# Kernel tuning notes

Hardware: AMD Instinct MI355X
Metric: run time of the kernel (lower is better)

## Reference

```python
import jax, jax.numpy as jnp
import numpy as np

B, T, IN = 128, 512, 3          # batch, stroke seq len, (dx,dy,pen)
A, H = 77, 512                  # alphabet size, hidden size
KW, KM, U = 10, 20, 64          # window mixtures, MDN mixtures, char seq len
OUT = 6 * KM + 1                # MDN output size


def setup_inputs() -> dict:
    key = jax.random.key(0)
    ks = jax.random.split(key, 16)
    p = lambda k, *sh: (jax.random.normal(k, sh, jnp.float32) * 0.05)
    in1 = IN + A            # lstm1 input: [x_t, w_prev]
    in2 = IN + A + H        # lstm2 input: [x_t, w_t, h1]
    return dict(
        x=jax.random.normal(ks[0], (B, T, IN), jnp.float32),
        c_seq=jax.random.uniform(ks[1], (B, U, A), jnp.float32),
        Wih1=p(ks[2], 4 * H, in1), Whh1=p(ks[3], 4 * H, H),
        bih1=p(ks[4], 4 * H), bhh1=p(ks[5], 4 * H),
        Wih2=p(ks[6], 4 * H, in2), Whh2=p(ks[7], 4 * H, H),
        bih2=p(ks[8], 4 * H), bhh2=p(ks[9], 4 * H),
        W_abk=p(ks[10], 3 * KW, H), b_abk=p(ks[11], 3 * KW),
        W_fc2=p(ks[12], OUT, H), b_fc2=p(ks[13], OUT),
    )


def _lstm_cell(xt, h, c, Wih, Whh, bih, bhh):
    # torch gate order: i, f, g, o
    z = xt @ Wih.T + h @ Whh.T + bih + bhh
    i, f, g, o = jnp.split(z, 4, axis=-1)
    c_new = jax.nn.sigmoid(f) * c + jax.nn.sigmoid(i) * jnp.tanh(g)
    h_new = jax.nn.sigmoid(o) * jnp.tanh(c_new)
    return h_new, c_new


def reference(x, c_seq, Wih1, Whh1, bih1, bhh1, Wih2, Whh2, bih2, bhh2,
              W_abk, b_abk, W_fc2, b_fc2):
    Bsz = x.shape[0]
    u = jnp.arange(c_seq.shape[1], dtype=jnp.float32)  # [U]

    def step(carry, x_t):
        h1, c1, h2, c2, kappa, w_pre = carry
        # first LSTM on [x_t, w_{t-1}]
        h1, c1 = _lstm_cell(jnp.concatenate([x_t, w_pre], -1), h1, c1,
                            Wih1, Whh1, bih1, bhh1)
        # attention window params
        abk = h1 @ W_abk.T + b_abk
        a_hat, b_hat, k_hat = jnp.split(abk, 3, axis=-1)
        alpha, beta = jnp.exp(a_hat), jnp.exp(b_hat)
        kappa = kappa + jnp.exp(k_hat)
        # phi[b,u] = sum_k alpha * exp(-beta * (kappa - u)^2)
        phi = jnp.sum(alpha[:, None, :] *
                      jnp.exp(-beta[:, None, :] *
                              (kappa[:, None, :] - u[None, :, None]) ** 2),
                      axis=2)                      # [B, U]
        w_t = jnp.einsum('bu,bua->ba', phi, c_seq)  # [B, A]
        # second LSTM on [x_t, w_t, h1]
        h2, c2 = _lstm_cell(jnp.concatenate([x_t, w_t, h1], -1), h2, c2,
                            Wih2, Whh2, bih2, bhh2)
        out = h2 @ W_fc2.T + b_fc2                  # [B, OUT]
        return (h1, c1, h2, c2, kappa, w_t), out

    z = lambda *sh: jnp.zeros(sh, x.dtype)
    carry0 = (z(Bsz, H), z(Bsz, H), z(Bsz, H), z(Bsz, H),
              z(Bsz, KW), z(Bsz, A))
    _, outs = jax.lax.scan(step, carry0, jnp.swapaxes(x, 0, 1))
    outs = jnp.swapaxes(outs, 0, 1)                 # [B, T, OUT]

    # MixtureDensityLayer
    K = KM
    pi = jax.nn.softmax(outs[..., :K], axis=-1)
    mu1 = outs[..., K:2 * K]
    mu2 = outs[..., 2 * K:3 * K]
    std1 = jnp.exp(outs[..., 3 * K:4 * K])
    std2 = jnp.exp(outs[..., 4 * K:5 * K])
    corr = jnp.tanh(outs[..., 5 * K:6 * K])
    eot = jax.nn.sigmoid(outs[..., -1:])
    return (pi, mu1, mu2, std1, std2, corr, eot)
```

## Files before the change

kernel.cpp:

```cpp
#include <hip/hip_runtime.h>
#include <math.h>

#define BB   128
#define TT   512
#define INX  3
#define AA   77
#define HH   512
#define KWD  10
#define KMD  20
#define UU   64
#define OUTD 121
#define IN1  80
#define IN2  592

#define MT   8
#define NJ   16
#define GRT  (HH/NJ)
#define MTL  (BB/MT)

#define PC1  596
#define PC3  1108

#define BH   (BB*HH)
#define BA   (BB*AA)
#define BKW  (BB*KWD)

__device__ __forceinline__ float sigf(float x) { return 1.0f / (1.0f + expf(-x)); }

__device__ __forceinline__ float dot4(float4 w, float4 a) {
    return w.x * a.x + w.y * a.y + w.z * a.z + w.w * a.w;
}

__device__ __forceinline__ void fc2_post(const float* __restrict__ h2r,
                                         const float* __restrict__ W_fc2,
                                         const float* __restrict__ b_fc2,
                                         float* __restrict__ out,
                                         int brow, int tprev, int tid,
                                         float* sY, float* sRed)
{
    if (tid < OUTD) {
        const float4* wr = (const float4*)(W_fc2 + (size_t)tid * HH);
        const float4* hv = (const float4*)h2r;
        float acc = b_fc2[tid];
#pragma unroll 4
        for (int k = 0; k < HH / 4; ++k)
            acc += dot4(wr[k], hv[k]);
        sY[tid] = acc;
    }
    __syncthreads();
    if (tid == 0) {
        float mx = sY[0];
        for (int i = 1; i < KMD; ++i) mx = fmaxf(mx, sY[i]);
        float s = 0.f;
        for (int i = 0; i < KMD; ++i) s += expf(sY[i] - mx);
        sRed[0] = mx; sRed[1] = s;
    }
    __syncthreads();
    if (tid < OUTD) {
        const size_t SZ = (size_t)BB * TT * KMD;
        const size_t bt = (size_t)brow * TT + tprev;
        float y = sY[tid];
        if      (tid <     KMD) out[             bt * KMD + tid          ] = expf(y - sRed[0]) / sRed[1];
        else if (tid < 2 * KMD) out[    SZ +     bt * KMD + (tid -   KMD)] = y;
        else if (tid < 3 * KMD) out[2 * SZ +     bt * KMD + (tid - 2*KMD)] = y;
        else if (tid < 4 * KMD) out[3 * SZ +     bt * KMD + (tid - 3*KMD)] = expf(y);
        else if (tid < 5 * KMD) out[4 * SZ +     bt * KMD + (tid - 4*KMD)] = expf(y);
        else if (tid < 6 * KMD) out[5 * SZ +     bt * KMD + (tid - 5*KMD)] = tanhf(y);
        else                    out[6 * SZ + bt] = sigf(y);
    }
}

__global__ __launch_bounds__(512, 4) void k1(
    const float* __restrict__ x,
    const float* __restrict__ Wih1, const float* __restrict__ Whh1,
    const float* __restrict__ bih1, const float* __restrict__ bhh1,
    const float* __restrict__ W_fc2, const float* __restrict__ b_fc2,
    const float* __restrict__ h1_old, float* __restrict__ h1_new,
    float* __restrict__ c1,
    const float* __restrict__ w_pre, const float* __restrict__ h2_prev,
    float* __restrict__ out, int t)
{
    __shared__ float sCat[MT][PC1];
    __shared__ float sZp[4][MT][68];
    __shared__ float sY[OUTD];
    __shared__ float sRed[2];

    const int tid  = threadIdx.x;
    const int grt  = blockIdx.x;
    const int mtl  = blockIdx.y;
    const int row0 = mtl * MT, unit0 = grt * NJ;

    {
        const int r = tid >> 6, c = tid & 63;
        const int b = row0 + r;
        const float4* s1 = (const float4*)(h1_old + (size_t)b * HH);
        float4* d1 = (float4*)&sCat[r][IN1];
        for (int i = c; i < HH / 4; i += 64) d1[i] = s1[i];
        for (int i = c; i < IN1; i += 64)
            sCat[r][i] = (i < INX) ? x[((size_t)b * TT + t) * INX + i]
                                   : w_pre[(size_t)b * AA + (i - INX)];
    }
    __syncthreads();

    {
        const int m = tid & 7, j = (tid >> 3) & 15, kq = tid >> 7;
        const int i0 = kq * 37, i1 = i0 + 37;
        const int u = unit0 + j;
        float a0 = 0.f, a1 = 0.f, a2 = 0.f, a3 = 0.f;
        const float4* sc = (const float4*)&sCat[m][0];

        const float4* w0a = (const float4*)Wih1 + (size_t)u * 20;
        const float4* w1a = (const float4*)Wih1 + (size_t)(HH + u) * 20;
        const float4* w2a = (const float4*)Wih1 + (size_t)(2 * HH + u) * 20;
        const float4* w3a = (const float4*)Wih1 + (size_t)(3 * HH + u) * 20;
        const int aEnd = (i1 < 20) ? i1 : 20;
        for (int i = i0; i < aEnd; ++i) {
            float4 a = sc[i];
            a0 += dot4(w0a[i], a); a1 += dot4(w1a[i], a);
            a2 += dot4(w2a[i], a); a3 += dot4(w3a[i], a);
        }
        const float4* w0b = (const float4*)Whh1 + (size_t)u * 128;
        const float4* w1b = (const float4*)Whh1 + (size_t)(HH + u) * 128;
        const float4* w2b = (const float4*)Whh1 + (size_t)(2 * HH + u) * 128;
        const float4* w3b = (const float4*)Whh1 + (size_t)(3 * HH + u) * 128;
        const int bSt = (i0 > 20) ? i0 : 20;
#pragma unroll 4
        for (int i = bSt; i < i1; ++i) {
            float4 a = sc[i];
            const int k = i - 20;
            a0 += dot4(w0b[k], a); a1 += dot4(w1b[k], a);
            a2 += dot4(w2b[k], a); a3 += dot4(w3b[k], a);
        }
        sZp[kq][m][j]      = a0;
        sZp[kq][m][16 + j] = a1;
        sZp[kq][m][32 + j] = a2;
        sZp[kq][m][48 + j] = a3;
    }
    __syncthreads();

    if (tid < MT * NJ) {
        const int m = tid >> 4, j = tid & 15;
        const int u = unit0 + j;
        float z[4];
#pragma unroll
        for (int g = 0; g < 4; ++g) {
            const int wr = g * HH + u;
            z[g] = bih1[wr] + bhh1[wr]
                 + sZp[0][m][g * 16 + j] + sZp[1][m][g * 16 + j]
                 + sZp[2][m][g * 16 + j] + sZp[3][m][g * 16 + j];
        }
        const size_t gi = (size_t)(row0 + m) * HH + u;
        const float cold = c1[gi];
        const float cn = sigf(z[1]) * cold + sigf(z[0]) * tanhf(z[2]);
        c1[gi] = cn;
        h1_new[gi] = sigf(z[3]) * tanhf(cn);
    }

    if (t > 0 && grt < MT) {
        const int brow = row0 + grt;
        fc2_post(h2_prev + (size_t)brow * HH, W_fc2, b_fc2, out, brow, t - 1, tid, sY, sRed);
    }
}

__global__ __launch_bounds__(256) void k2(
    const float* __restrict__ c_seq,
    const float* __restrict__ W_abk, const float* __restrict__ b_abk,
    const float* __restrict__ h1_cur,
    const float* __restrict__ kap_old, float* __restrict__ kap_new,
    float* __restrict__ w_new)
{
    __shared__ float sH1[HH];
    __shared__ float sAbk[32];
    __shared__ float sAl[KWD], sBe[KWD], sKa[KWD];
    __shared__ float sPhi[UU];

    const int tid = threadIdx.x;
    const int b   = blockIdx.x;

    if (tid < HH / 4)
        ((float4*)sH1)[tid] = ((const float4*)(h1_cur + (size_t)b * HH))[tid];
    __syncthreads();

    {
        const int o = tid >> 3, kk = tid & 7;
        float acc = 0.f;
        if (o < 3 * KWD) {
            const float4* wp = (const float4*)(W_abk + (size_t)o * HH) + kk * 16;
            const float4* hp = (const float4*)sH1 + kk * 16;
#pragma unroll
            for (int k = 0; k < 16; ++k)
                acc += dot4(wp[k], hp[k]);
        }
        acc += __shfl_xor(acc, 1);
        acc += __shfl_xor(acc, 2);
        acc += __shfl_xor(acc, 4);
        if (o < 3 * KWD && kk == 0) sAbk[o] = acc + b_abk[o];
    }
    __syncthreads();

    if (tid < KWD) {
        const float al = expf(sAbk[tid]);
        const float be = expf(sAbk[KWD + tid]);
        const float ka = kap_old[(size_t)b * KWD + tid] + expf(sAbk[2 * KWD + tid]);
        sAl[tid] = al; sBe[tid] = be; sKa[tid] = ka;
        kap_new[(size_t)b * KWD + tid] = ka;
    }
    __syncthreads();

    if (tid < UU) {
        const float u = (float)tid;
        float s = 0.f;
#pragma unroll
        for (int k = 0; k < KWD; ++k) {
            const float d = sKa[k] - u;
            s += sAl[k] * expf(-sBe[k] * d * d);
        }
        sPhi[tid] = s;
    }
    __syncthreads();

    if (tid < AA) {
        float s = 0.f;
        const float* cp = c_seq + (size_t)b * UU * AA + tid;
#pragma unroll 4
        for (int u = 0; u < UU; ++u) s += sPhi[u] * cp[(size_t)u * AA];
        w_new[(size_t)b * AA + tid] = s;
    }
}

__global__ __launch_bounds__(512, 4) void k3(
    const float* __restrict__ x,
    const float* __restrict__ Wih2, const float* __restrict__ Whh2,
    const float* __restrict__ bih2, const float* __restrict__ bhh2,
    const float* __restrict__ h1_cur, const float* __restrict__ w_cur,
    const float* __restrict__ h2_old, float* __restrict__ h2_new,
    float* __restrict__ c2, int t)
{
    __shared__ float sCat[MT][PC3];
    __shared__ float sZp[4][MT][68];

    const int tid  = threadIdx.x;
    const int grt  = blockIdx.x;
    const int mtl  = blockIdx.y;
    const int row0 = mtl * MT, unit0 = grt * NJ;

    {
        const int r = tid >> 6, c = tid & 63;
        const int b = row0 + r;
        const float4* s1 = (const float4*)(h1_cur + (size_t)b * HH);
        const float4* s2 = (const float4*)(h2_old + (size_t)b * HH);
        float4* d1 = (float4*)&sCat[r][IN1];
        float4* d2 = (float4*)&sCat[r][IN2];
        for (int i = c; i < HH / 4; i += 64) { d1[i] = s1[i]; d2[i] = s2[i]; }
        for (int i = c; i < IN1; i += 64)
            sCat[r][i] = (i < INX) ? x[((size_t)b * TT + t) * INX + i]
                                   : w_cur[(size_t)b * AA + (i - INX)];
    }
    __syncthreads();

    {
        const int m = tid & 7, j = (tid >> 3) & 15, kq = tid >> 7;
        const int i0 = kq * 69, i1 = i0 + 69;
        const int u = unit0 + j;
        float a0 = 0.f, a1 = 0.f, a2 = 0.f, a3 = 0.f;
        const float4* sc = (const float4*)&sCat[m][0];

        const float4* w0a = (const float4*)Wih2 + (size_t)u * 148;
        const float4* w1a = (const float4*)Wih2 + (size_t)(HH + u) * 148;
        const float4* w2a = (const float4*)Wih2 + (size_t)(2 * HH + u) * 148;
        const float4* w3a = (const float4*)Wih2 + (size_t)(3 * HH + u) * 148;
        const int aEnd = (i1 < 148) ? i1 : 148;
#pragma unroll 4
        for (int i = i0; i < aEnd; ++i) {
            float4 a = sc[i];
            a0 += dot4(w0a[i], a); a1 += dot4(w1a[i], a);
            a2 += dot4(w2a[i], a); a3 += dot4(w3a[i], a);
        }
        const float4* w0b = (const float4*)Whh2 + (size_t)u * 128;
        const float4* w1b = (const float4*)Whh2 + (size_t)(HH + u) * 128;
        const float4* w2b = (const float4*)Whh2 + (size_t)(2 * HH + u) * 128;
        const float4* w3b = (const float4*)Whh2 + (size_t)(3 * HH + u) * 128;
        const int bSt = (i0 > 148) ? i0 : 148;
#pragma unroll 4
        for (int i = bSt; i < i1; ++i) {
            float4 a = sc[i];
            const int k = i - 148;
            a0 += dot4(w0b[k], a); a1 += dot4(w1b[k], a);
            a2 += dot4(w2b[k], a); a3 += dot4(w3b[k], a);
        }
        sZp[kq][m][j]      = a0;
        sZp[kq][m][16 + j] = a1;
        sZp[kq][m][32 + j] = a2;
        sZp[kq][m][48 + j] = a3;
    }
    __syncthreads();

    if (tid < MT * NJ) {
        const int m = tid >> 4, j = tid & 15;
        const int u = unit0 + j;
        float z[4];
#pragma unroll
        for (int g = 0; g < 4; ++g) {
            const int wr = g * HH + u;
            z[g] = bih2[wr] + bhh2[wr]
                 + sZp[0][m][g * 16 + j] + sZp[1][m][g * 16 + j]
                 + sZp[2][m][g * 16 + j] + sZp[3][m][g * 16 + j];
        }
        const size_t gi = (size_t)(row0 + m) * HH + u;
        const float cold = c2[gi];
        const float cn = sigf(z[1]) * cold + sigf(z[0]) * tanhf(z[2]);
        c2[gi] = cn;
        h2_new[gi] = sigf(z[3]) * tanhf(cn);
    }
}

__global__ __launch_bounds__(128) void fc2_final(
    const float* __restrict__ h2_last,
    const float* __restrict__ W_fc2, const float* __restrict__ b_fc2,
    float* __restrict__ out)
{
    __shared__ float sY[OUTD];
    __shared__ float sRed[2];
    const int brow = blockIdx.x;
    fc2_post(h2_last + (size_t)brow * HH, W_fc2, b_fc2, out, brow, TT - 1, threadIdx.x, sY, sRed);
}

extern "C" void kernel_launch(void* const* d_in, const int* in_sizes, int n_in,
                              void* d_out, int out_size, void* d_ws, size_t ws_size,
                              hipStream_t stream) {
    const float* x     = (const float*)d_in[0];
    const float* c_seq = (const float*)d_in[1];
    const float* Wih1  = (const float*)d_in[2];
    const float* Whh1  = (const float*)d_in[3];
    const float* bih1  = (const float*)d_in[4];
    const float* bhh1  = (const float*)d_in[5];
    const float* Wih2  = (const float*)d_in[6];
    const float* Whh2  = (const float*)d_in[7];
    const float* bih2  = (const float*)d_in[8];
    const float* bhh2  = (const float*)d_in[9];
    const float* W_abk = (const float*)d_in[10];
    const float* b_abk = (const float*)d_in[11];
    const float* W_fc2 = (const float*)d_in[12];
    const float* b_fc2 = (const float*)d_in[13];
    float* out = (float*)d_out;

    float* ws  = (float*)d_ws;
    float* h1b = ws;
    float* h2b = ws + 2 * BH;
    float* c1  = ws + 4 * BH;
    float* c2  = ws + 5 * BH;
    float* kap = ws + 6 * BH;
    float* wb  = ws + 6 * BH + 2 * BKW;
    const size_t used = (size_t)6 * BH + 2 * BKW + 2 * BA;

    hipMemsetAsync(d_ws, 0, used * sizeof(float), stream);

    const dim3 grid(GRT, MTL), blk(512);
    for (int t = 0; t < TT; ++t) {
        const int p = t & 1;
        k1<<<grid, blk, 0, stream>>>(x, Wih1, Whh1, bih1, bhh1, W_fc2, b_fc2,
                                     h1b + (size_t)p * BH, h1b + (size_t)(1 - p) * BH, c1,
                                     wb + (size_t)p * BA, h2b + (size_t)p * BH, out, t);
        k2<<<dim3(BB), dim3(256), 0, stream>>>(c_seq, W_abk, b_abk,
                                               h1b + (size_t)(1 - p) * BH,
                                               kap + (size_t)p * BKW, kap + (size_t)(1 - p) * BKW,
                                               wb + (size_t)(1 - p) * BA);
        k3<<<grid, blk, 0, stream>>>(x, Wih2, Whh2, bih2, bhh2,
                                     h1b + (size_t)(1 - p) * BH, wb + (size_t)(1 - p) * BA,
                                     h2b + (size_t)p * BH, h2b + (size_t)(1 - p) * BH, c2, t);
    }
    fc2_final<<<dim3(BB), dim3(128), 0, stream>>>(h2b, W_fc2, b_fc2, out);
}
```

Measured before the change: 43.82 ms.

## Fuse per-timestep LSTM kernels into one persistent cooperative kernel with grid syncs

Replaces the three kernel launches per timestep (LSTM1, attention, LSTM2) with a single cooperative persistent kernel. It loops over all timesteps and separates the phases with grid-wide syncs, which removes about 1500 kernel launches and their launch gaps. Work-groups shrink from 512 to 256 threads, each splitting the K reduction two ways instead of four, so two groups can sit on each CU. If the cooperative launch fails, it falls back to the multi-launch path. The cost is grid-barrier latency and lower per-group parallelism in the gate matvecs.

```diff
diff --git a/kernel.cpp b/kernel.cpp
--- a/kernel.cpp
+++ b/kernel.cpp
@@ -1,5 +1,8 @@
 #include <hip/hip_runtime.h>
+#include <hip/hip_cooperative_groups.h>
 #include <math.h>
+
+namespace cg = cooperative_groups;
 
 #define BB   128
 #define TT   512
@@ -17,6 +20,7 @@
 #define NJ   16
 #define GRT  (HH/NJ)
 #define MTL  (BB/MT)
+#define NWG  (GRT*MTL)
 
 #define PC1  596
 #define PC3  1108
@@ -70,44 +74,33 @@
     }
 }
 
-__global__ __launch_bounds__(512, 4) void k1(
+__device__ __forceinline__ void lstm1_body(
     const float* __restrict__ x,
     const float* __restrict__ Wih1, const float* __restrict__ Whh1,
     const float* __restrict__ bih1, const float* __restrict__ bhh1,
-    const float* __restrict__ W_fc2, const float* __restrict__ b_fc2,
     const float* __restrict__ h1_old, float* __restrict__ h1_new,
-    float* __restrict__ c1,
-    const float* __restrict__ w_pre, const float* __restrict__ h2_prev,
-    float* __restrict__ out, int t)
-{
-    __shared__ float sCat[MT][PC1];
-    __shared__ float sZp[4][MT][68];
-    __shared__ float sY[OUTD];
-    __shared__ float sRed[2];
-
-    const int tid  = threadIdx.x;
-    const int grt  = blockIdx.x;
-    const int mtl  = blockIdx.y;
+    float* __restrict__ c1, const float* __restrict__ w_pre,
+    int t, int tid, int grt, int mtl, float* sCat, float* sZp)
+{
     const int row0 = mtl * MT, unit0 = grt * NJ;
-
     {
-        const int r = tid >> 6, c = tid & 63;
+        const int r = tid >> 5, cc = tid & 31;
         const int b = row0 + r;
+        float* rowp = sCat + r * PC1;
         const float4* s1 = (const float4*)(h1_old + (size_t)b * HH);
-        float4* d1 = (float4*)&sCat[r][IN1];
-        for (int i = c; i < HH / 4; i += 64) d1[i] = s1[i];
-        for (int i = c; i < IN1; i += 64)
-            sCat[r][i] = (i < INX) ? x[((size_t)b * TT + t) * INX + i]
-                                   : w_pre[(size_t)b * AA + (i - INX)];
-    }
-    __syncthreads();
-
+        float4* d1 = (float4*)(rowp + IN1);
+        for (int i = cc; i < HH / 4; i += 32) d1[i] = s1[i];
+        for (int i = cc; i < IN1; i += 32)
+            rowp[i] = (i < INX) ? x[((size_t)b * TT + t) * INX + i]
+                                : w_pre[(size_t)b * AA + (i - INX)];
+    }
+    __syncthreads();
     {
         const int m = tid & 7, j = (tid >> 3) & 15, kq = tid >> 7;
-        const int i0 = kq * 37, i1 = i0 + 37;
+        const int i0 = kq * 74, i1 = i0 + 74;
         const int u = unit0 + j;
         float a0 = 0.f, a1 = 0.f, a2 = 0.f, a3 = 0.f;
-        const float4* sc = (const float4*)&sCat[m][0];
+        const float4* sc = (const float4*)(sCat + m * PC1);
 
         const float4* w0a = (const float4*)Wih1 + (size_t)u * 20;
         const float4* w1a = (const float4*)Wih1 + (size_t)(HH + u) * 20;
@@ -131,23 +124,23 @@
             a0 += dot4(w0b[k], a); a1 += dot4(w1b[k], a);
             a2 += dot4(w2b[k], a); a3 += dot4(w3b[k], a);
         }
-        sZp[kq][m][j]      = a0;
-        sZp[kq][m][16 + j] = a1;
-        sZp[kq][m][32 + j] = a2;
-        sZp[kq][m][48 + j] = a3;
-    }
-    __syncthreads();
-
+        float* zr = sZp + ((kq << 3) | m) * 68;
+        zr[j]      = a0;
+        zr[16 + j] = a1;
+        zr[32 + j] = a2;
+        zr[48 + j] = a3;
+    }
+    __syncthreads();
     if (tid < MT * NJ) {
         const int m = tid >> 4, j = tid & 15;
         const int u = unit0 + j;
+        const float* z0 = sZp + m * 68;
+        const float* z1 = sZp + (8 + m) * 68;
         float z[4];
 #pragma unroll
         for (int g = 0; g < 4; ++g) {
             const int wr = g * HH + u;
-            z[g] = bih1[wr] + bhh1[wr]
-                 + sZp[0][m][g * 16 + j] + sZp[1][m][g * 16 + j]
-                 + sZp[2][m][g * 16 + j] + sZp[3][m][g * 16 + j];
+            z[g] = bih1[wr] + bhh1[wr] + z0[g * 16 + j] + z1[g * 16 + j];
         }
         const size_t gi = (size_t)(row0 + m) * HH + u;
         const float cold = c1[gi];
@@ -155,115 +148,38 @@
         c1[gi] = cn;
         h1_new[gi] = sigf(z[3]) * tanhf(cn);
     }
-
-    if (t > 0 && grt < MT) {
-        const int brow = row0 + grt;
-        fc2_post(h2_prev + (size_t)brow * HH, W_fc2, b_fc2, out, brow, t - 1, tid, sY, sRed);
-    }
-}
-
-__global__ __launch_bounds__(256) void k2(
-    const float* __restrict__ c_seq,
-    const float* __restrict__ W_abk, const float* __restrict__ b_abk,
-    const float* __restrict__ h1_cur,
-    const float* __restrict__ kap_old, float* __restrict__ kap_new,
-    float* __restrict__ w_new)
-{
-    __shared__ float sH1[HH];
-    __shared__ float sAbk[32];
-    __shared__ float sAl[KWD], sBe[KWD], sKa[KWD];
-    __shared__ float sPhi[UU];
-
-    const int tid = threadIdx.x;
-    const int b   = blockIdx.x;
-
-    if (tid < HH / 4)
-        ((float4*)sH1)[tid] = ((const float4*)(h1_cur + (size_t)b * HH))[tid];
-    __syncthreads();
-
-    {
-        const int o = tid >> 3, kk = tid & 7;
-        float acc = 0.f;
-        if (o < 3 * KWD) {
-            const float4* wp = (const float4*)(W_abk + (size_t)o * HH) + kk * 16;
-            const float4* hp = (const float4*)sH1 + kk * 16;
-#pragma unroll
-            for (int k = 0; k < 16; ++k)
-                acc += dot4(wp[k], hp[k]);
-        }
-        acc += __shfl_xor(acc, 1);
-        acc += __shfl_xor(acc, 2);
-        acc += __shfl_xor(acc, 4);
-        if (o < 3 * KWD && kk == 0) sAbk[o] = acc + b_abk[o];
-    }
-    __syncthreads();
-
-    if (tid < KWD) {
-        const float al = expf(sAbk[tid]);
-        const float be = expf(sAbk[KWD + tid]);
-        const float ka = kap_old[(size_t)b * KWD + tid] + expf(sAbk[2 * KWD + tid]);
-        sAl[tid] = al; sBe[tid] = be; sKa[tid] = ka;
-        kap_new[(size_t)b * KWD + tid] = ka;
-    }
-    __syncthreads();
-
-    if (tid < UU) {
-        const float u = (float)tid;
-        float s = 0.f;
-#pragma unroll
-        for (int k = 0; k < KWD; ++k) {
-            const float d = sKa[k] - u;
-            s += sAl[k] * expf(-sBe[k] * d * d);
-        }
-        sPhi[tid] = s;
-    }
-    __syncthreads();
-
-    if (tid < AA) {
-        float s = 0.f;
-        const float* cp = c_seq + (size_t)b * UU * AA + tid;
-#pragma unroll 4
-        for (int u = 0; u < UU; ++u) s += sPhi[u] * cp[(size_t)u * AA];
-        w_new[(size_t)b * AA + tid] = s;
-    }
-}
-
-__global__ __launch_bounds__(512, 4) void k3(
+}
+
+__device__ __forceinline__ void lstm2_body(
     const float* __restrict__ x,
     const float* __restrict__ Wih2, const float* __restrict__ Whh2,
     const float* __restrict__ bih2, const float* __restrict__ bhh2,
     const float* __restrict__ h1_cur, const float* __restrict__ w_cur,
     const float* __restrict__ h2_old, float* __restrict__ h2_new,
-    float* __restrict__ c2, int t)
-{
-    __shared__ float sCat[MT][PC3];
-    __shared__ float sZp[4][MT][68];
-
-    const int tid  = threadIdx.x;
-    const int grt  = blockIdx.x;
-    const int mtl  = blockIdx.y;
+    float* __restrict__ c2,
+    int t, int tid, int grt, int mtl, float* sCat, float* sZp)
+{
     const int row0 = mtl * MT, unit0 = grt * NJ;
-
     {
-        const int r = tid >> 6, c = tid & 63;
+        const int r = tid >> 5, cc = tid & 31;
         const int b = row0 + r;
+        float* rowp = sCat + r * PC3;
         const float4* s1 = (const float4*)(h1_cur + (size_t)b * HH);
         const float4* s2 = (const float4*)(h2_old + (size_t)b * HH);
-        float4* d1 = (float4*)&sCat[r][IN1];
-        float4* d2 = (float4*)&sCat[r][IN2];
-        for (int i = c; i < HH / 4; i += 64) { d1[i] = s1[i]; d2[i] = s2[i]; }
-        for (int i = c; i < IN1; i += 64)
-            sCat[r][i] = (i < INX) ? x[((size_t)b * TT + t) * INX + i]
-                                   : w_cur[(size_t)b * AA + (i - INX)];
-    }
-    __syncthreads();
-
+        float4* d1 = (float4*)(rowp + IN1);
+        float4* d2 = (float4*)(rowp + IN2);
+        for (int i = cc; i < HH / 4; i += 32) { d1[i] = s1[i]; d2[i] = s2[i]; }
+        for (int i = cc; i < IN1; i += 32)
+            rowp[i] = (i < INX) ? x[((size_t)b * TT + t) * INX + i]
+                                : w_cur[(size_t)b * AA + (i - INX)];
+    }
+    __syncthreads();
     {
         const int m = tid & 7, j = (tid >> 3) & 15, kq = tid >> 7;
-        const int i0 = kq * 69, i1 = i0 + 69;
+        const int i0 = kq * 138, i1 = i0 + 138;
         const int u = unit0 + j;
         float a0 = 0.f, a1 = 0.f, a2 = 0.f, a3 = 0.f;
-        const float4* sc = (const float4*)&sCat[m][0];
+        const float4* sc = (const float4*)(sCat + m * PC3);
 
         const float4* w0a = (const float4*)Wih2 + (size_t)u * 148;
         const float4* w1a = (const float4*)Wih2 + (size_t)(HH + u) * 148;
@@ -288,23 +204,23 @@
             a0 += dot4(w0b[k], a); a1 += dot4(w1b[k], a);
             a2 += dot4(w2b[k], a); a3 += dot4(w3b[k], a);
         }
-        sZp[kq][m][j]      = a0;
-        sZp[kq][m][16 + j] = a1;
-        sZp[kq][m][32 + j] = a2;
-        sZp[kq][m][48 + j] = a3;
-    }
-    __syncthreads();
-
+        float* zr = sZp + ((kq << 3) | m) * 68;
+        zr[j]      = a0;
+        zr[16 + j] = a1;
+        zr[32 + j] = a2;
+        zr[48 + j] = a3;
+    }
+    __syncthreads();
     if (tid < MT * NJ) {
         const int m = tid >> 4, j = tid & 15;
         const int u = unit0 + j;
+        const float* z0 = sZp + m * 68;
+        const float* z1 = sZp + (8 + m) * 68;
         float z[4];
 #pragma unroll
         for (int g = 0; g < 4; ++g) {
             const int wr = g * HH + u;
-            z[g] = bih2[wr] + bhh2[wr]
-                 + sZp[0][m][g * 16 + j] + sZp[1][m][g * 16 + j]
-                 + sZp[2][m][g * 16 + j] + sZp[3][m][g * 16 + j];
+            z[g] = bih2[wr] + bhh2[wr] + z0[g * 16 + j] + z1[g * 16 + j];
         }
         const size_t gi = (size_t)(row0 + m) * HH + u;
         const float cold = c2[gi];
@@ -314,15 +230,183 @@
     }
 }
 
+__device__ __forceinline__ void attn_body(
+    const float* __restrict__ c_seq,
+    const float* __restrict__ W_abk, const float* __restrict__ b_abk,
+    const float* __restrict__ h1_cur,
+    const float* __restrict__ kap_old, float* __restrict__ kap_new,
+    float* __restrict__ w_new, int b, int tid, float* sH1, float* zf)
+{
+    float* sAbk = zf;
+    float* sAl  = zf + 32;
+    float* sBe  = zf + 48;
+    float* sKa  = zf + 64;
+    float* sPhi = zf + 80;
+
+    if (tid < HH / 4)
+        ((float4*)sH1)[tid] = ((const float4*)(h1_cur + (size_t)b * HH))[tid];
+    __syncthreads();
+
+    {
+        const int o = tid >> 3, kk = tid & 7;
+        float acc = 0.f;
+        if (o < 3 * KWD) {
+            const float4* wp = (const float4*)(W_abk + (size_t)o * HH) + kk * 16;
+            const float4* hp = (const float4*)sH1 + kk * 16;
+#pragma unroll
+            for (int k = 0; k < 16; ++k)
+                acc += dot4(wp[k], hp[k]);
+        }
+        acc += __shfl_xor(acc, 1);
+        acc += __shfl_xor(acc, 2);
+        acc += __shfl_xor(acc, 4);
+        if (o < 3 * KWD && kk == 0) sAbk[o] = acc + b_abk[o];
+    }
+    __syncthreads();
+
+    if (tid < KWD) {
+        const float al = expf(sAbk[tid]);
+        const float be = expf(sAbk[KWD + tid]);
+        const float ka = kap_old[(size_t)b * KWD + tid] + expf(sAbk[2 * KWD + tid]);
+        sAl[tid] = al; sBe[tid] = be; sKa[tid] = ka;
+        kap_new[(size_t)b * KWD + tid] = ka;
+    }
+    __syncthreads();
+
+    if (tid < UU) {
+        const float u = (float)tid;
+        float s = 0.f;
+#pragma unroll
+        for (int k = 0; k < KWD; ++k) {
+            const float d = sKa[k] - u;
+            s += sAl[k] * expf(-sBe[k] * d * d);
+        }
+        sPhi[tid] = s;
+    }
+    __syncthreads();
+
+    if (tid < AA) {
+        float s = 0.f;
+        const float* cp = c_seq + (size_t)b * UU * AA + tid;
+#pragma unroll 4
+        for (int u = 0; u < UU; ++u) s += sPhi[u] * cp[(size_t)u * AA];
+        w_new[(size_t)b * AA + tid] = s;
+    }
+}
+
+__global__ __launch_bounds__(256, 2) void fused(
+    const float* __restrict__ x, const float* __restrict__ c_seq,
+    const float* __restrict__ Wih1, const float* __restrict__ Whh1,
+    const float* __restrict__ bih1, const float* __restrict__ bhh1,
+    const float* __restrict__ Wih2, const float* __restrict__ Whh2,
+    const float* __restrict__ bih2, const float* __restrict__ bhh2,
+    const float* __restrict__ W_abk, const float* __restrict__ b_abk,
+    const float* __restrict__ W_fc2, const float* __restrict__ b_fc2,
+    float* __restrict__ h1b, float* __restrict__ h2b,
+    float* __restrict__ c1, float* __restrict__ c2,
+    float* __restrict__ kapb, float* __restrict__ wbuf,
+    float* __restrict__ out)
+{
+    __shared__ float sCat[MT * PC3];
+    __shared__ float sZp[2 * MT * 68];
+    __shared__ float sAux[OUTD + 8];
+
+    const int tid = threadIdx.x;
+    const int wg  = blockIdx.x;
+    const int grt = wg & 31, mtl = wg >> 5;
+    cg::grid_group gg = cg::this_grid();
+
+    for (int t = 0; t < TT; ++t) {
+        const int p = t & 1;
+        const float* h1_old  = h1b  + (size_t)p * BH;
+        float*       h1_new  = h1b  + (size_t)(1 - p) * BH;
+        const float* h2_old  = h2b  + (size_t)p * BH;
+        float*       h2_new  = h2b  + (size_t)(1 - p) * BH;
+        const float* w_pre   = wbuf + (size_t)p * BA;
+        float*       w_new   = wbuf + (size_t)(1 - p) * BA;
+        const float* kap_old = kapb + (size_t)p * BKW;
+        float*       kap_new = kapb + (size_t)(1 - p) * BKW;
+
+        lstm1_body(x, Wih1, Whh1, bih1, bhh1, h1_old, h1_new, c1, w_pre,
+                   t, tid, grt, mtl, sCat, sZp);
+        gg.sync();
+
+        if (wg < BB) {
+            attn_body(c_seq, W_abk, b_abk, h1_new, kap_old, kap_new, w_new,
+                      wg, tid, sCat, sZp);
+        } else if (wg < 2 * BB) {
+            if (t > 0)
+                fc2_post(h2_old + (size_t)(wg - BB) * HH, W_fc2, b_fc2, out,
+                         wg - BB, t - 1, tid, sAux, sAux + OUTD);
+        }
+        gg.sync();
+
+        lstm2_body(x, Wih2, Whh2, bih2, bhh2, h1_new, w_new, h2_old, h2_new, c2,
+                   t, tid, grt, mtl, sCat, sZp);
+    }
+
+    gg.sync();
+    if (wg < BB)
+        fc2_post(h2b + (size_t)wg * HH, W_fc2, b_fc2, out, wg, TT - 1, tid,
+                 sAux, sAux + OUTD);
+}
+
+__global__ __launch_bounds__(256) void k1(
+    const float* __restrict__ x,
+    const float* __restrict__ Wih1, const float* __restrict__ Whh1,
+    const float* __restrict__ bih1, const float* __restrict__ bhh1,
+    const float* __restrict__ W_fc2, const float* __restrict__ b_fc2,
+    const float* __restrict__ h1_old, float* __restrict__ h1_new,
+    float* __restrict__ c1,
+    const float* __restrict__ w_pre, const float* __restrict__ h2_prev,
+    float* __restrict__ out, int t)
+{
+    __shared__ float sCat[MT * PC1];
+    __shared__ float sZp[2 * MT * 68];
+    __shared__ float sAux[OUTD + 8];
+    const int tid = threadIdx.x, grt = blockIdx.x, mtl = blockIdx.y;
+    lstm1_body(x, Wih1, Whh1, bih1, bhh1, h1_old, h1_new, c1, w_pre,
+               t, tid, grt, mtl, sCat, sZp);
+    if (t > 0 && grt < MT)
+        fc2_post(h2_prev + (size_t)(mtl * MT + grt) * HH, W_fc2, b_fc2, out,
+                 mtl * MT + grt, t - 1, tid, sAux, sAux + OUTD);
+}
+
+__global__ __launch_bounds__(256) void k2(
+    const float* __restrict__ c_seq,
+    const float* __restrict__ W_abk, const float* __restrict__ b_abk,
+    const float* __restrict__ h1_cur,
+    const float* __restrict__ kap_old, float* __restrict__ kap_new,
+    float* __restrict__ w_new)
+{
+    __shared__ float sH1[HH];
+    __shared__ float zf[160];
+    attn_body(c_seq, W_abk, b_abk, h1_cur, kap_old, kap_new, w_new,
+              blockIdx.x, threadIdx.x, sH1, zf);
+}
+
+__global__ __launch_bounds__(256) void k3(
+    const float* __restrict__ x,
+    const float* __restrict__ Wih2, const float* __restrict__ Whh2,
+    const float* __restrict__ bih2, const float* __restrict__ bhh2,
+    const float* __restrict__ h1_cur, const float* __restrict__ w_cur,
+    const float* __restrict__ h2_old, float* __restrict__ h2_new,
+    float* __restrict__ c2, int t)
+{
+    __shared__ float sCat[MT * PC3];
+    __shared__ float sZp[2 * MT * 68];
+    lstm2_body(x, Wih2, Whh2, bih2, bhh2, h1_cur, w_cur, h2_old, h2_new, c2,
+               t, threadIdx.x, blockIdx.x, blockIdx.y, sCat, sZp);
+}
+
 __global__ __launch_bounds__(128) void fc2_final(
     const float* __restrict__ h2_last,
     const float* __restrict__ W_fc2, const float* __restrict__ b_fc2,
     float* __restrict__ out)
 {
-    __shared__ float sY[OUTD];
-    __shared__ float sRed[2];
-    const int brow = blockIdx.x;
-    fc2_post(h2_last + (size_t)brow * HH, W_fc2, b_fc2, out, brow, TT - 1, threadIdx.x, sY, sRed);
+    __shared__ float sAux[OUTD + 8];
+    fc2_post(h2_last + (size_t)blockIdx.x * HH, W_fc2, b_fc2, out,
+             blockIdx.x, TT - 1, threadIdx.x, sAux, sAux + OUTD);
 }
 
 extern "C" void kernel_launch(void* const* d_in, const int* in_sizes, int n_in,
@@ -355,19 +439,32 @@
 
     hipMemsetAsync(d_ws, 0, used * sizeof(float), stream);
 
-    const dim3 grid(GRT, MTL), blk(512);
-    for (int t = 0; t < TT; ++t) {
-        const int p = t & 1;
-        k1<<<grid, blk, 0, stream>>>(x, Wih1, Whh1, bih1, bhh1, W_fc2, b_fc2,
-                                     h1b + (size_t)p * BH, h1b + (size_t)(1 - p) * BH, c1,
-                                     wb + (size_t)p * BA, h2b + (size_t)p * BH, out, t);
-        k2<<<dim3(BB), dim3(256), 0, stream>>>(c_seq, W_abk, b_abk,
-                                               h1b + (size_t)(1 - p) * BH,
-                                               kap + (size_t)p * BKW, kap + (size_t)(1 - p) * BKW,
-                                               wb + (size_t)(1 - p) * BA);
-        k3<<<grid, blk, 0, stream>>>(x, Wih2, Whh2, bih2, bhh2,
-                                     h1b + (size_t)(1 - p) * BH, wb + (size_t)(1 - p) * BA,
-                                     h2b + (size_t)p * BH, h2b + (size_t)(1 - p) * BH, c2, t);
-    }
-    fc2_final<<<dim3(BB), dim3(128), 0, stream>>>(h2b, W_fc2, b_fc2, out);
-}
+    void* args[] = {
+        (void*)&x, (void*)&c_seq,
+        (void*)&Wih1, (void*)&Whh1, (void*)&bih1, (void*)&bhh1,
+        (void*)&Wih2, (void*)&Whh2, (void*)&bih2, (void*)&bhh2,
+        (void*)&W_abk, (void*)&b_abk, (void*)&W_fc2, (void*)&b_fc2,
+        (void*)&h1b, (void*)&h2b, (void*)&c1, (void*)&c2,
+        (void*)&kap, (void*)&wb, (void*)&out
+    };
+    hipError_t err = hipLaunchCooperativeKernel((const void*)fused, dim3(NWG),
+                                                dim3(256), args, 0, stream);
+    if (err != hipSuccess) {
+        (void)hipGetLastError();
+        const dim3 grid(GRT, MTL), blk(256);
+        for (int t = 0; t < TT; ++t) {
+            const int p = t & 1;
+            k1<<<grid, blk, 0, stream>>>(x, Wih1, Whh1, bih1, bhh1, W_fc2, b_fc2,
+                                         h1b + (size_t)p * BH, h1b + (size_t)(1 - p) * BH, c1,
+                                         wb + (size_t)p * BA, h2b + (size_t)p * BH, out, t);
+            k2<<<dim3(BB), blk, 0, stream>>>(c_seq, W_abk, b_abk,
+                                             h1b + (size_t)(1 - p) * BH,
+                                             kap + (size_t)p * BKW, kap + (size_t)(1 - p) * BKW,
+                                             wb + (size_t)(1 - p) * BA);
+            k3<<<grid, blk, 0, stream>>>(x, Wih2, Whh2, bih2, bhh2,
+                                         h1b + (size_t)(1 - p) * BH, wb + (size_t)(1 - p) * BA,
+                                         h2b + (size_t)p * BH, h2b + (size_t)(1 - p) * BH, c2, t);
+        }
+        fc2_final<<<dim3(BB), dim3(128), 0, stream>>>(h2b, W_fc2, b_fc2, out);
+    }
+}
```

Result: slower. 92.40 ms (+110.8%).
